# Performance work log

Hardware: AMD Instinct MI355X
Metric: run time of the kernel (lower is better)

## Reference

```python
import jax, jax.numpy as jnp
import numpy as np

B, S = 2, 1024
V, H = 32000, 1024
NH, NKV = 16, 8
HD = H // NH          # 64
L = 8
I = 4 * H             # 4096
EPS = 1e-6
THETA = 10000.0
NEG = -1e9


def setup_inputs() -> dict:
    key = jax.random.key(0)
    ks = jax.random.split(key, 12)
    std = 0.02
    f = lambda k, shape: jax.random.normal(k, shape, jnp.float32) * std
    return {
        "input_ids": jax.random.randint(ks[0], (B, S), 0, V, dtype=jnp.int32),
        "embed": f(ks[1], (V, H)),
        "Wq": f(ks[2], (L, H, NH * HD)),
        "Wk": f(ks[3], (L, H, NKV * HD)),
        "Wv": f(ks[4], (L, H, NKV * HD)),
        "Wo": f(ks[5], (L, NH * HD, H)),
        "Wg": f(ks[6], (L, H, I)),
        "Wu": f(ks[7], (L, H, I)),
        "Wd": f(ks[8], (L, I, H)),
        "ln1": jnp.ones((L, H), jnp.float32),
        "ln2": jnp.ones((L, H), jnp.float32),
        "norm_w": jnp.ones((H,), jnp.float32),
        "lm_head": f(ks[9], (H, V)),
    }


def _rmsnorm(x, w):
    var = jnp.mean(x * x, axis=-1, keepdims=True)
    return x * jax.lax.rsqrt(var + EPS) * w


def _rotate_half(x):
    x1, x2 = jnp.split(x, 2, axis=-1)
    return jnp.concatenate((-x2, x1), axis=-1)


def reference(input_ids, embed, Wq, Wk, Wv, Wo, Wg, Wu, Wd, ln1, ln2, norm_w, lm_head):
    # RoPE tables [S, HD] (freqs duplicated, matching cat((freqs, freqs)))
    inv_freq = 1.0 / (THETA ** (jnp.arange(0, HD, 2, dtype=jnp.float32) / HD))
    t = jnp.arange(S, dtype=jnp.float32)
    freqs = t[:, None] * inv_freq[None, :]
    emb = jnp.concatenate((freqs, freqs), axis=-1)
    cos = jnp.cos(emb)[None, None]  # [1,1,S,HD]
    sin = jnp.sin(emb)[None, None]
    # causal mask [S, S]
    mask = jnp.where(jnp.tril(jnp.ones((S, S), bool)), 0.0, NEG).astype(jnp.float32)

    def layer(h, p):
        wq, wk, wv, wo, wg, wu, wd, g1, g2 = p
        x = _rmsnorm(h, g1)
        q = (x @ wq).reshape(B, S, NH, HD).transpose(0, 2, 1, 3)   # [B,NH,S,HD]
        k = (x @ wk).reshape(B, S, NKV, HD).transpose(0, 2, 1, 3)  # [B,NKV,S,HD]
        v = (x @ wv).reshape(B, S, NKV, HD).transpose(0, 2, 1, 3)
        q = q * cos + _rotate_half(q) * sin
        k = k * cos + _rotate_half(k) * sin
        rep = NH // NKV
        k = jnp.repeat(k, rep, axis=1)  # GQA repeat_interleave
        v = jnp.repeat(v, rep, axis=1)
        scores = jnp.einsum("bhqd,bhkd->bhqk", q, k) / np.sqrt(HD) + mask
        probs = jax.nn.softmax(scores, axis=-1)
        o = jnp.einsum("bhqk,bhkd->bhqd", probs, v)
        o = o.transpose(0, 2, 1, 3).reshape(B, S, NH * HD)
        h = h + o @ wo
        x = _rmsnorm(h, g2)
        h = h + (jax.nn.silu(x @ wg) * (x @ wu)) @ wd
        return h, None

    h = embed[input_ids]  # [B,S,H]
    h, _ = jax.lax.scan(layer, h, (Wq, Wk, Wv, Wo, Wg, Wu, Wd, ln1, ln2))
    h = _rmsnorm(h, norm_w)
    return h @ lm_head  # logits [B,S,V]
```

## Files before the change

kernel.cpp:

```cpp
#include <hip/hip_runtime.h>


typedef unsigned short u16;
typedef __bf16  bf16x8 __attribute__((ext_vector_type(8)));
typedef unsigned short u16x8 __attribute__((ext_vector_type(8)));
typedef float   f32x4  __attribute__((ext_vector_type(4)));

#define DEV static __device__ __forceinline__

constexpr int NB  = 2;
constexpr int S   = 1024;
constexpr int NT  = NB * S;
constexpr int H   = 1024;
constexpr int NH  = 16;
constexpr int NKV = 8;
constexpr int HD  = 64;
constexpr int NL  = 8;
constexpr int FF  = 4096;
constexpr int V   = 32000;
constexpr int QKVW = 2048;

DEV float b2f(u16 x) { return __uint_as_float(((unsigned)x) << 16); }
DEV u16   f2b(float f) {
  unsigned i = __float_as_uint(f);
  return (u16)((i + 0x7fffu + ((i >> 16) & 1u)) >> 16);
}

DEV void gload16(const void* g, void* l) {
  __builtin_amdgcn_global_load_lds(
      (const __attribute__((address_space(1))) void*)g,
      (__attribute__((address_space(3))) void*)l, 16, 0, 0);
}

DEV bf16x8 ld128(const u16* p) { return *reinterpret_cast<const bf16x8*>(p); }

template <int EPI>
__global__ __launch_bounds__(512, 2) void gemm256_k(
    const u16* __restrict__ A, int lda,
    const u16* __restrict__ Bt, int ldb,
    void* __restrict__ C, int ldc, int K)
{
  __shared__ __align__(16) u16 Asm[4][256 * 32];
  __shared__ __align__(16) u16 Bsm[4][256 * 32];

  const int tid  = threadIdx.x;
  const int lane = tid & 63;
  const int lrow = lane & 15;
  const int g    = lane >> 4;
  const int wid  = tid >> 6;
  const int wm   = wid >> 2, wn = wid & 3;

  int flat = blockIdx.y * gridDim.x + blockIdx.x;
  const int cpx = (gridDim.x * gridDim.y) >> 3;
  flat = (flat & 7) * cpx + (flat >> 3);
  const int bx = flat % gridDim.x;
  const int by = flat / gridDim.x;

  const int r0   = tid >> 2, pp = tid & 3;
  const int row1 = 128 + (tid >> 2);
  const int p0 = pp ^ ((r0 ^ (r0 >> 2)) & 3);
  const int p1 = pp ^ ((row1 ^ (row1 >> 2)) & 3);
  const u16* aS0 = A  + (size_t)(bx * 256 + r0)   * lda + p0 * 8;
  const u16* aS1 = A  + (size_t)(bx * 256 + row1) * lda + p1 * 8;
  const u16* bS0 = Bt + (size_t)(by * 256 + r0)   * ldb + p0 * 8;
  const u16* bS1 = Bt + (size_t)(by * 256 + row1) * ldb + p1 * 8;
  const int aB0 = tid * 16, aB1 = (512 + tid) * 16;

  int aOff[8], bOff[4];
  #pragma unroll
  for (int fm = 0; fm < 8; fm++) {
    const int r = wm * 128 + fm * 16 + lrow;
    aOff[fm] = r * 32 + (g ^ ((r ^ (r >> 2)) & 3)) * 8;
  }
  #pragma unroll
  for (int fn = 0; fn < 4; fn++) {
    const int r = wn * 64 + fn * 16 + lrow;
    bOff[fn] = r * 32 + (g ^ ((r ^ (r >> 2)) & 3)) * 8;
  }

  f32x4 acc[8][4] = {};
  const int ntk = K / 32;

  #pragma unroll
  for (int ts = 0; ts < 3; ts++) {
    const long kt = (long)ts * 32;
    gload16(aS0 + kt, (char*)Asm[ts] + aB0);
    gload16(bS0 + kt, (char*)Bsm[ts] + aB0);
    gload16(aS1 + kt, (char*)Asm[ts] + aB1);
    gload16(bS1 + kt, (char*)Bsm[ts] + aB1);
  }
  asm volatile("s_waitcnt vmcnt(8)" ::: "memory");
  __builtin_amdgcn_s_barrier();

#define KTILE(VMW, STG)                                                         \
  {                                                                             \
    const int rs = t & 3, ss = (t + 3) & 3;                                     \
    const long kt = (long)(t + 3) * 32;                                         \
    bf16x8 af[4], bf[4];                                                        \
    _Pragma("unroll") for (int i = 0; i < 4; i++) bf[i] = ld128(&Bsm[rs][bOff[i]]); \
    _Pragma("unroll") for (int i = 0; i < 4; i++) af[i] = ld128(&Asm[rs][aOff[i]]); \
    if (STG) { gload16(aS0 + kt, (char*)Asm[ss] + aB0);                         \
               gload16(bS0 + kt, (char*)Bsm[ss] + aB0); }                       \
    __builtin_amdgcn_s_barrier();                                               \
    asm volatile("s_waitcnt lgkmcnt(0)" ::: "memory");                          \
    __builtin_amdgcn_sched_barrier(0);                                          \
    __builtin_amdgcn_s_setprio(1);                                              \
    _Pragma("unroll") for (int m = 0; m < 4; m++)                               \
      _Pragma("unroll") for (int n = 0; n < 4; n++)                             \
        acc[m][n] = __builtin_amdgcn_mfma_f32_16x16x32_bf16(af[m], bf[n], acc[m][n], 0, 0, 0); \
    __builtin_amdgcn_s_setprio(0);                                              \
    __builtin_amdgcn_s_barrier();                                               \
    _Pragma("unroll") for (int i = 0; i < 4; i++) af[i] = ld128(&Asm[rs][aOff[4 + i]]); \
    if (STG) { gload16(aS1 + kt, (char*)Asm[ss] + aB1);                         \
               gload16(bS1 + kt, (char*)Bsm[ss] + aB1); }                       \
    __builtin_amdgcn_s_barrier();                                               \
    asm volatile("s_waitcnt lgkmcnt(0)" ::: "memory");                          \
    __builtin_amdgcn_sched_barrier(0);                                          \
    __builtin_amdgcn_s_setprio(1);                                              \
    _Pragma("unroll") for (int m = 0; m < 4; m++)                               \
      _Pragma("unroll") for (int n = 0; n < 4; n++)                             \
        acc[4 + m][n] = __builtin_amdgcn_mfma_f32_16x16x32_bf16(af[m], bf[n], acc[4 + m][n], 0, 0, 0); \
    __builtin_amdgcn_s_setprio(0);                                              \
    VMW;                                                                        \
    __builtin_amdgcn_sched_barrier(0);                                          \
    __builtin_amdgcn_s_barrier();                                               \
  }

  {
    int t = 0;
    for (; t < ntk - 3; ++t) KTILE(asm volatile("s_waitcnt vmcnt(8)" ::: "memory"), true);
    KTILE(asm volatile("s_waitcnt vmcnt(4)" ::: "memory"), false); ++t;
    KTILE(asm volatile("s_waitcnt vmcnt(0)" ::: "memory"), false); ++t;
    KTILE((void)0, false);
  }
#undef KTILE

  if (EPI == 2) {
    #pragma unroll
    for (int fm = 0; fm < 8; fm++) {
      #pragma unroll
      for (int fp = 0; fp < 2; fp++) {
        #pragma unroll
        for (int r = 0; r < 4; r++) {
          const size_t row = bx * 256 + wm * 128 + fm * 16 + g * 4 + r;
          const int nb = by * 256 + wn * 64 + fp * 32;
          const int oc = (nb >> 5) * 16 + lrow;
          const float gg = acc[fm][2 * fp][r];
          const float uu = acc[fm][2 * fp + 1][r];
          ((u16*)C)[row * ldc + oc] = f2b(gg / (1.f + __expf(-gg)) * uu);
        }
      }
    }
  } else {
    #pragma unroll
    for (int fm = 0; fm < 8; fm++) {
      #pragma unroll
      for (int fn = 0; fn < 4; fn++) {
        #pragma unroll
        for (int r = 0; r < 4; r++) {
          const size_t row = bx * 256 + wm * 128 + fm * 16 + g * 4 + r;
          const size_t col = by * 256 + wn * 64 + fn * 16 + lrow;
          ((float*)C)[row * ldc + col] = acc[fm][fn][r];
        }
      }
    }
  }
}

template <int BM, int BN, int WM, int WN, int EPI>
__global__ __launch_bounds__(256) void gemm_k(
    const u16* __restrict__ A, int lda,
    const u16* __restrict__ Bt, int ldb,
    void* __restrict__ C, int ldc,
    const float2* __restrict__ tab, int K)
{
  __shared__ __align__(16) u16 As[BM * 32];
  __shared__ __align__(16) u16 Bs[BN * 32];

  const int tid  = threadIdx.x;
  const int lane = tid & 63;
  const int lrow = lane & 15;
  const int kb   = lane >> 4;
  const int w    = tid >> 6;
  const int wm   = w / WN, wn = w % WN;
  constexpr int WR = BM / WM, WC = BN / WN;
  constexpr int FM = WR / 16, FN = WC / 16;

  const u16* Ap = A + blockIdx.x * BM * lda;
  const u16* Bp = Bt + blockIdx.y * BN * ldb;

  f32x4 acc[FM][FN] = {};

  for (int k0 = 0; k0 < K; k0 += 32) {
    #pragma unroll
    for (int i = 0; i < (BM * 4) / 256; i++) {
      const int c = i * 256 + tid;
      gload16(Ap + (c >> 2) * lda + k0 + (c & 3) * 8, (char*)As + c * 16);
    }
    #pragma unroll
    for (int i = 0; i < (BN * 4) / 256; i++) {
      const int c = i * 256 + tid;
      gload16(Bp + (c >> 2) * ldb + k0 + (c & 3) * 8, (char*)Bs + c * 16);
    }
    __syncthreads();

    bf16x8 af[FM], bfv[FN];
    #pragma unroll
    for (int fm = 0; fm < FM; fm++)
      af[fm] = *reinterpret_cast<const bf16x8*>(As + (wm * WR + fm * 16 + lrow) * 32 + kb * 8);
    #pragma unroll
    for (int fn = 0; fn < FN; fn++)
      bfv[fn] = *reinterpret_cast<const bf16x8*>(Bs + (wn * WC + fn * 16 + lrow) * 32 + kb * 8);

    #pragma unroll
    for (int fm = 0; fm < FM; fm++) {
      #pragma unroll
      for (int fn = 0; fn < FN; fn++) {
        acc[fm][fn] = __builtin_amdgcn_mfma_f32_16x16x32_bf16(af[fm], bfv[fn], acc[fm][fn], 0, 0, 0);
      }
    }
    __syncthreads();
  }

  if (EPI == 4) {
    const int colb = blockIdx.y * BN + wn * WC;
    const int head = colb >> 6;
    const float qs = (head < 16) ? 0.125f : 1.0f;
    #pragma unroll
    for (int fm = 0; fm < FM; fm++) {
      #pragma unroll
      for (int r = 0; r < 4; r++) {
        const int row = blockIdx.x * BM + wm * WR + fm * 16 + kb * 4 + r;
        if (head >= 24) {
          #pragma unroll
          for (int fn = 0; fn < FN; fn++)
            ((u16*)C)[row * ldc + colb + fn * 16 + lrow] = f2b(acc[fm][fn][r]);
        } else {
          const int s = row & (S - 1);
          #pragma unroll
          for (int fp = 0; fp < 2; fp++) {
            const int d = fp * 16 + lrow;
            const float2 cs = tab[s * 32 + d];
            const float x1 = acc[fm][fp][r];
            const float x2 = acc[fm][fp + 2][r];
            ((u16*)C)[row * ldc + colb + d]      = f2b((x1 * cs.x - x2 * cs.y) * qs);
            ((u16*)C)[row * ldc + colb + d + 32] = f2b((x2 * cs.x + x1 * cs.y) * qs);
          }
        }
      }
    }
  } else {
    #pragma unroll
    for (int fm = 0; fm < FM; fm++) {
      #pragma unroll
      for (int fn = 0; fn < FN; fn++) {
        #pragma unroll
        for (int r = 0; r < 4; r++) {
          const int row = blockIdx.x * BM + wm * WR + fm * 16 + kb * 4 + r;
          const int col = blockIdx.y * BN + wn * WC + fn * 16 + lrow;
          const float vv = acc[fm][fn][r];
          if (EPI == 0) ((u16*)C)[row * ldc + col] = f2b(vv);
          else          ((float*)C)[row * ldc + col] += vv;
        }
      }
    }
  }
}

__global__ __launch_bounds__(256) void transpose_k(
    const float* __restrict__ W, u16* __restrict__ WT, int K, int N, int rmode,
    size_t wstride, size_t tstride)
{
  __shared__ float t[32][33];
  const float* Wp = W + (size_t)blockIdx.z * wstride;
  u16* WTp = WT + (size_t)blockIdx.z * tstride;
  const int k0 = blockIdx.x * 32, n0 = blockIdx.y * 32;
  const int tx = threadIdx.x & 31, ty = threadIdx.x >> 5;
  #pragma unroll
  for (int i = 0; i < 32; i += 8)
    t[ty + i][tx] = Wp[(size_t)(k0 + ty + i) * N + (n0 + tx)];
  __syncthreads();
  #pragma unroll
  for (int i = 0; i < 32; i += 8) {
    const int n = n0 + ty + i;
    const int orow = (rmode == 0) ? n : ((n >> 4) * 32 + (n & 15) + ((rmode == 2) ? 16 : 0));
    WTp[(size_t)orow * K + (k0 + tx)] = f2b(t[tx][ty + i]);
  }
}

__global__ __launch_bounds__(256) void embed_k(
    const int* __restrict__ ids, const float* __restrict__ E, float* __restrict__ h)
{
  const int t = blockIdx.x;
  const int id = ids[t];
  ((float4*)(h + t * H))[threadIdx.x] = ((const float4*)(E + (size_t)id * H))[threadIdx.x];
}

__global__ __launch_bounds__(256) void rmsnorm_k(
    const float* __restrict__ h, const float* __restrict__ w, u16* __restrict__ x)
{
  const int row = blockIdx.x;
  const float4 hv = ((const float4*)(h + row * H))[threadIdx.x];
  float s = hv.x * hv.x + hv.y * hv.y + hv.z * hv.z + hv.w * hv.w;
  #pragma unroll
  for (int off = 32; off; off >>= 1) s += __shfl_xor(s, off, 64);
  __shared__ float red[4];
  if ((threadIdx.x & 63) == 0) red[threadIdx.x >> 6] = s;
  __syncthreads();
  s = red[0] + red[1] + red[2] + red[3];
  const float scale = rsqrtf(s * (1.f / H) + 1e-6f);
  const float4 wv = ((const float4*)w)[threadIdx.x];
  ushort4 ov;
  ov.x = f2b(hv.x * scale * wv.x);
  ov.y = f2b(hv.y * scale * wv.y);
  ov.z = f2b(hv.z * scale * wv.z);
  ov.w = f2b(hv.w * scale * wv.w);
  ((ushort4*)(x + row * H))[threadIdx.x] = ov;
}

__global__ __launch_bounds__(256) void ropetab_k(float2* __restrict__ tab)
{
  const int idx = blockIdx.x * 256 + threadIdx.x;
  const int s = idx >> 5, d = idx & 31;
  const float ang = s * powf(10000.f, -(2.f * d) / 64.f);
  float sn, cs;
  sincosf(ang, &sn, &cs);
  tab[idx] = make_float2(cs, sn);
}

__global__ __launch_bounds__(256) void fattn_k(
    const u16* __restrict__ qkv, u16* __restrict__ o)
{
  __shared__ __align__(16) u16 Ks[64 * 64];
  __shared__ __align__(16) u16 Vt[64 * 72];
  __shared__ __align__(16) u16 Pw[4][16 * 64];

  const int tid  = threadIdx.x;
  const int lane = tid & 63;
  const int lrow = lane & 15;
  const int g    = lane >> 4;
  const int w    = tid >> 6;
  const int bp = blockIdx.x, by = blockIdx.y;
  const int b = by >> 4, hh = by & 15, kh = hh >> 1;

  for (int half = 0; half < 2; half++) {
    const int bx = half ? (15 - bp) : bp;
    const int q0 = bx * 64;

    bf16x8 aq[2];
    {
      const int qrow = q0 + w * 16 + lrow;
      const u16* qp = qkv + (size_t)(b * S + qrow) * QKVW + hh * 64 + g * 8;
      aq[0] = *reinterpret_cast<const bf16x8*>(qp);
      aq[1] = *reinterpret_cast<const bf16x8*>(qp + 32);
    }

    f32x4 oacc[4] = {};
    float mrow[4], lsum[4];
    #pragma unroll
    for (int r = 0; r < 4; r++) { mrow[r] = -1e30f; lsum[r] = 0.f; }

    const int nt = bx + 1;
    for (int t = 0; t < nt; t++) {
      const int kv0 = t * 64;
      __syncthreads();

      #pragma unroll
      for (int i = 0; i < 2; i++) {
        const int c = i * 256 + tid;
        const int r = c >> 3, p = c & 7;
        gload16(qkv + (size_t)(b * S + kv0 + r) * QKVW + 1024 + kh * 64 + ((p ^ (r & 7)) * 8),
                (char*)Ks + c * 16);
      }
      u16x8 vreg[2];
      #pragma unroll
      for (int i = 0; i < 2; i++) {
        const int c = i * 256 + tid;
        const int k = c >> 3, dch = c & 7;
        vreg[i] = *reinterpret_cast<const u16x8*>(
            qkv + (size_t)(b * S + kv0 + k) * QKVW + 1536 + kh * 64 + dch * 8);
      }
      #pragma unroll
      for (int i = 0; i < 2; i++) {
        const int c = i * 256 + tid;
        const int k = c >> 3, d0 = (c & 7) * 8;
        #pragma unroll
        for (int j = 0; j < 8; j++) {
          const int d = d0 + j;
          Vt[d * 72 + (((k >> 3) ^ (d >> 3)) * 8) + (k & 7)] = vreg[i][j];
        }
      }
      __syncthreads();

      f32x4 sacc[4] = {};
      #pragma unroll
      for (int n = 0; n < 4; n++) {
        const int row = n * 16 + lrow;
        #pragma unroll
        for (int k2 = 0; k2 < 2; k2++) {
          const bf16x8 bk = *reinterpret_cast<const bf16x8*>(
              Ks + row * 64 + (((k2 * 4 + g) ^ (row & 7)) * 8));
          sacc[n] = __builtin_amdgcn_mfma_f32_16x16x32_bf16(aq[k2], bk, sacc[n], 0, 0, 0);
        }
      }

      #pragma unroll
      for (int r = 0; r < 4; r++) {
        const int qglob = q0 + w * 16 + g * 4 + r;
        float sv[4];
        float rm = -1e30f;
        #pragma unroll
        for (int n = 0; n < 4; n++) {
          const int kg = kv0 + n * 16 + lrow;
          sv[n] = (kg <= qglob) ? sacc[n][r] : -1e30f;
          rm = fmaxf(rm, sv[n]);
        }
        #pragma unroll
        for (int mk = 1; mk < 16; mk <<= 1) rm = fmaxf(rm, __shfl_xor(rm, mk, 64));
        const float mnew  = fmaxf(mrow[r], rm);
        const float scale = __expf(mrow[r] - mnew);
        float rs = 0.f;
        u16 pb[4];
        #pragma unroll
        for (int n = 0; n < 4; n++) {
          const float p = __expf(sv[n] - mnew);
          rs += p;
          pb[n] = f2b(p);
        }
        #pragma unroll
        for (int mk = 1; mk < 16; mk <<= 1) rs += __shfl_xor(rs, mk, 64);
        lsum[r] = lsum[r] * scale + rs;
        mrow[r] = mnew;
        #pragma unroll
        for (int dt = 0; dt < 4; dt++) oacc[dt][r] *= scale;
        const int ql = g * 4 + r;
        #pragma unroll
        for (int n = 0; n < 4; n++) {
          const int k = n * 16 + lrow;
          Pw[w][ql * 64 + (((k >> 3) ^ (ql & 7)) * 8) + (k & 7)] = pb[n];
        }
      }

      #pragma unroll
      for (int k2 = 0; k2 < 2; k2++) {
        const bf16x8 pa = *reinterpret_cast<const bf16x8*>(
            &Pw[w][lrow * 64 + (((k2 * 4 + g) ^ (lrow & 7)) * 8)]);
        #pragma unroll
        for (int dt = 0; dt < 4; dt++) {
          const int d = dt * 16 + lrow;
          const bf16x8 vb = *reinterpret_cast<const bf16x8*>(
              &Vt[d * 72 + (((k2 * 4 + g) ^ (d >> 3)) * 8)]);
          oacc[dt] = __builtin_amdgcn_mfma_f32_16x16x32_bf16(pa, vb, oacc[dt], 0, 0, 0);
        }
      }
    }

    #pragma unroll
    for (int dt = 0; dt < 4; dt++) {
      #pragma unroll
      for (int r = 0; r < 4; r++) {
        const int qrow = q0 + w * 16 + g * 4 + r;
        o[(size_t)(b * S + qrow) * H + hh * 64 + dt * 16 + lrow] =
            f2b(oacc[dt][r] / lsum[r]);
      }
    }
  }
}

extern "C" void kernel_launch(void* const* d_in, const int* in_sizes, int n_in,
                              void* d_out, int out_size, void* d_ws, size_t ws_size,
                              hipStream_t stream)
{
  const int*   ids  = (const int*)d_in[0];
  const float* EW   = (const float*)d_in[1];
  const float* Wq   = (const float*)d_in[2];
  const float* Wk   = (const float*)d_in[3];
  const float* Wv   = (const float*)d_in[4];
  const float* Wo   = (const float*)d_in[5];
  const float* Wg   = (const float*)d_in[6];
  const float* Wu   = (const float*)d_in[7];
  const float* Wd   = (const float*)d_in[8];
  const float* ln1  = (const float*)d_in[9];
  const float* ln2  = (const float*)d_in[10];
  const float* nw   = (const float*)d_in[11];
  const float* lmw  = (const float*)d_in[12];
  float* out = (float*)d_out;

  const size_t MB = 1u << 20;
  char* ws = (char*)d_ws;
  float*  h   = (float*)(ws);
  u16*    x   = (u16*)(ws + 8 * MB);
  u16*    qkv = (u16*)(ws + 12 * MB);
  u16*    o   = (u16*)(ws + 20 * MB);
  u16*    ub  = (u16*)(ws + 24 * MB);
  float2* tab = (float2*)(ws + 40 * MB);
  char*   wb  = ws + 41 * MB;

  const size_t sqkv = (size_t)QKVW * H;
  const size_t swo  = (size_t)H * H;
  const size_t sgu  = (size_t)2 * FF * H;
  const size_t swd  = (size_t)H * FF;

  const bool full = ws_size >= 345 * MB;
  if (!full && ws_size < 104 * MB) return;

  u16 *wqkvT, *woT, *wguT, *wdT, *lmT;
  if (full) {
    wqkvT = (u16*)wb;
    woT   = wqkvT + NL * sqkv;
    wguT  = woT + NL * swo;
    wdT   = wguT + NL * sgu;
    lmT   = wdT + NL * swd;
  } else {
    wqkvT = (u16*)wb;
    woT   = wqkvT + sqkv;
    wguT  = woT + swo;
    wdT   = wguT + sgu;
    lmT   = (u16*)wb;
  }

  auto xpose = [&](int l0, int lz, bool dense) {
    const size_t tq = dense ? sqkv : 0, to = dense ? swo : 0;
    const size_t tg = dense ? sgu : 0,  td = dense ? swd : 0;
    transpose_k<<<dim3(H / 32, H / 32, lz), 256, 0, stream>>>(
        Wq + (size_t)l0 * H * H, wqkvT + (size_t)l0 * tq, H, H, 0, (size_t)H * H, tq);
    transpose_k<<<dim3(H / 32, 512 / 32, lz), 256, 0, stream>>>(
        Wk + (size_t)l0 * H * 512, wqkvT + (size_t)l0 * tq + (size_t)1024 * H, H, 512, 0,
        (size_t)H * 512, tq);
    transpose_k<<<dim3(H / 32, 512 / 32, lz), 256, 0, stream>>>(
        Wv + (size_t)l0 * H * 512, wqkvT + (size_t)l0 * tq + (size_t)1536 * H, H, 512, 0,
        (size_t)H * 512, tq);
    transpose_k<<<dim3(H / 32, H / 32, lz), 256, 0, stream>>>(
        Wo + (size_t)l0 * H * H, woT + (size_t)l0 * to, H, H, 0, (size_t)H * H, to);
    transpose_k<<<dim3(H / 32, FF / 32, lz), 256, 0, stream>>>(
        Wg + (size_t)l0 * H * FF, wguT + (size_t)l0 * tg, H, FF, 1, (size_t)H * FF, tg);
    transpose_k<<<dim3(H / 32, FF / 32, lz), 256, 0, stream>>>(
        Wu + (size_t)l0 * H * FF, wguT + (size_t)l0 * tg, H, FF, 2, (size_t)H * FF, tg);
    transpose_k<<<dim3(FF / 32, H / 32, lz), 256, 0, stream>>>(
        Wd + (size_t)l0 * FF * H, wdT + (size_t)l0 * td, FF, H, 0, (size_t)FF * H, td);
  };

  embed_k<<<NT, 256, 0, stream>>>(ids, EW, h);
  ropetab_k<<<(S * 32) / 256, 256, 0, stream>>>(tab);

  if (full) {
    xpose(0, NL, true);
    transpose_k<<<dim3(H / 32, V / 32, 1), 256, 0, stream>>>(lmw, lmT, H, V, 0, 0, 0);
  }

  for (int l = 0; l < NL; l++) {
    if (!full) xpose(l, 1, false);
    u16* pq = wqkvT + (full ? (size_t)l * sqkv : 0);
    u16* po = woT   + (full ? (size_t)l * swo  : 0);
    u16* pg = wguT  + (full ? (size_t)l * sgu  : 0);
    u16* pd = wdT   + (full ? (size_t)l * swd  : 0);

    rmsnorm_k<<<NT, 256, 0, stream>>>(h, ln1 + l * H, x);
    gemm_k<64, 256, 1, 4, 4><<<dim3(NT / 64, QKVW / 256), 256, 0, stream>>>(
        x, H, pq, H, qkv, QKVW, tab, H);
    fattn_k<<<dim3(8, NB * NH), 256, 0, stream>>>(qkv, o);
    gemm_k<64, 128, 1, 4, 1><<<dim3(NT / 64, H / 128), 256, 0, stream>>>(
        o, H, po, H, h, H, nullptr, H);

    rmsnorm_k<<<NT, 256, 0, stream>>>(h, ln2 + l * H, x);
    gemm256_k<2><<<dim3(NT / 256, (2 * FF) / 256), 512, 0, stream>>>(
        x, H, pg, H, ub, FF, H);
    gemm_k<64, 128, 1, 4, 1><<<dim3(NT / 64, H / 128), 256, 0, stream>>>(
        ub, FF, pd, FF, h, H, nullptr, FF);
  }

  rmsnorm_k<<<NT, 256, 0, stream>>>(h, nw, x);
  if (!full)
    transpose_k<<<dim3(H / 32, V / 32, 1), 256, 0, stream>>>(lmw, lmT, H, V, 0, 0, 0);
  gemm256_k<3><<<dim3(NT / 256, V / 256), 512, 0, stream>>>(
      x, H, lmT, H, out, V, H);
}
```

Before: 2.254 ms.

## Fuse residual add into RMSNorm and retile projection GEMMs

The Wo and Wd projection GEMMs now write a bf16 delta buffer instead of read-modify-writing the fp32 residual. A new addnorm kernel adds that delta to the residual and computes the next RMSNorm in one pass, which removes the separate rmsnorm launches and the extra read of h. The GEMM tile shapes change to 64x64 and 64x128 with a different warp layout, giving more blocks on these narrow GEMMs. The trade-off is rounding the residual delta to bf16 before accumulation, plus a slightly larger workspace.

```diff
diff --git a/kernel.cpp b/kernel.cpp
--- a/kernel.cpp
+++ b/kernel.cpp
@@ -258,9 +258,7 @@
         for (int r = 0; r < 4; r++) {
           const int row = blockIdx.x * BM + wm * WR + fm * 16 + kb * 4 + r;
           const int col = blockIdx.y * BN + wn * WC + fn * 16 + lrow;
-          const float vv = acc[fm][fn][r];
-          if (EPI == 0) ((u16*)C)[row * ldc + col] = f2b(vv);
-          else          ((float*)C)[row * ldc + col] += vv;
+          ((u16*)C)[row * ldc + col] = f2b(acc[fm][fn][r]);
         }
       }
     }
@@ -318,6 +316,32 @@
   ((ushort4*)(x + row * H))[threadIdx.x] = ov;
 }
 
+__global__ __launch_bounds__(256) void addnorm_k(
+    float* __restrict__ h, const u16* __restrict__ dl,
+    const float* __restrict__ w, u16* __restrict__ x)
+{
+  const int row = blockIdx.x;
+  float4 hv = ((const float4*)(h + row * H))[threadIdx.x];
+  const ushort4 dv = ((const ushort4*)(dl + row * H))[threadIdx.x];
+  hv.x += b2f(dv.x); hv.y += b2f(dv.y); hv.z += b2f(dv.z); hv.w += b2f(dv.w);
+  ((float4*)(h + row * H))[threadIdx.x] = hv;
+  float s = hv.x * hv.x + hv.y * hv.y + hv.z * hv.z + hv.w * hv.w;
+  #pragma unroll
+  for (int off = 32; off; off >>= 1) s += __shfl_xor(s, off, 64);
+  __shared__ float red[4];
+  if ((threadIdx.x & 63) == 0) red[threadIdx.x >> 6] = s;
+  __syncthreads();
+  s = red[0] + red[1] + red[2] + red[3];
+  const float scale = rsqrtf(s * (1.f / H) + 1e-6f);
+  const float4 wv = ((const float4*)w)[threadIdx.x];
+  ushort4 ov;
+  ov.x = f2b(hv.x * scale * wv.x);
+  ov.y = f2b(hv.y * scale * wv.y);
+  ov.z = f2b(hv.z * scale * wv.z);
+  ov.w = f2b(hv.w * scale * wv.w);
+  ((ushort4*)(x + row * H))[threadIdx.x] = ov;
+}
+
 __global__ __launch_bounds__(256) void ropetab_k(float2* __restrict__ tab)
 {
   const int idx = blockIdx.x * 256 + threadIdx.x;
@@ -492,17 +516,18 @@
   u16*    x   = (u16*)(ws + 8 * MB);
   u16*    qkv = (u16*)(ws + 12 * MB);
   u16*    o   = (u16*)(ws + 20 * MB);
-  u16*    ub  = (u16*)(ws + 24 * MB);
-  float2* tab = (float2*)(ws + 40 * MB);
-  char*   wb  = ws + 41 * MB;
+  u16*    dl  = (u16*)(ws + 24 * MB);
+  u16*    ub  = (u16*)(ws + 28 * MB);
+  float2* tab = (float2*)(ws + 44 * MB);
+  char*   wb  = ws + 45 * MB;
 
   const size_t sqkv = (size_t)QKVW * H;
   const size_t swo  = (size_t)H * H;
   const size_t sgu  = (size_t)2 * FF * H;
   const size_t swd  = (size_t)H * FF;
 
-  const bool full = ws_size >= 345 * MB;
-  if (!full && ws_size < 104 * MB) return;
+  const bool full = ws_size >= 349 * MB;
+  if (!full && ws_size < 108 * MB) return;
 
   u16 *wqkvT, *woT, *wguT, *wdT, *lmT;
   if (full) {
@@ -548,6 +573,8 @@
     transpose_k<<<dim3(H / 32, V / 32, 1), 256, 0, stream>>>(lmw, lmT, H, V, 0, 0, 0);
   }
 
+  rmsnorm_k<<<NT, 256, 0, stream>>>(h, ln1, x);
+
   for (int l = 0; l < NL; l++) {
     if (!full) xpose(l, 1, false);
     u16* pq = wqkvT + (full ? (size_t)l * sqkv : 0);
@@ -555,21 +582,21 @@
     u16* pg = wguT  + (full ? (size_t)l * sgu  : 0);
     u16* pd = wdT   + (full ? (size_t)l * swd  : 0);
 
-    rmsnorm_k<<<NT, 256, 0, stream>>>(h, ln1 + l * H, x);
-    gemm_k<64, 256, 1, 4, 4><<<dim3(NT / 64, QKVW / 256), 256, 0, stream>>>(
+    gemm_k<64, 128, 2, 2, 4><<<dim3(NT / 64, QKVW / 128), 256, 0, stream>>>(
         x, H, pq, H, qkv, QKVW, tab, H);
     fattn_k<<<dim3(8, NB * NH), 256, 0, stream>>>(qkv, o);
-    gemm_k<64, 128, 1, 4, 1><<<dim3(NT / 64, H / 128), 256, 0, stream>>>(
-        o, H, po, H, h, H, nullptr, H);
-
-    rmsnorm_k<<<NT, 256, 0, stream>>>(h, ln2 + l * H, x);
+    gemm_k<64, 64, 2, 2, 0><<<dim3(NT / 64, H / 64), 256, 0, stream>>>(
+        o, H, po, H, dl, H, nullptr, H);
+    addnorm_k<<<NT, 256, 0, stream>>>(h, dl, ln2 + l * H, x);
+
     gemm256_k<2><<<dim3(NT / 256, (2 * FF) / 256), 512, 0, stream>>>(
         x, H, pg, H, ub, FF, H);
-    gemm_k<64, 128, 1, 4, 1><<<dim3(NT / 64, H / 128), 256, 0, stream>>>(
-        ub, FF, pd, FF, h, H, nullptr, FF);
-  }
-
-  rmsnorm_k<<<NT, 256, 0, stream>>>(h, nw, x);
+    gemm_k<64, 64, 2, 2, 0><<<dim3(NT / 64, H / 64), 256, 0, stream>>>(
+        ub, FF, pd, FF, dl, H, nullptr, FF);
+    const float* nxt = (l + 1 < NL) ? (ln1 + (l + 1) * H) : nw;
+    addnorm_k<<<NT, 256, 0, stream>>>(h, dl, nxt, x);
+  }
+
   if (!full)
     transpose_k<<<dim3(H / 32, V / 32, 1), 256, 0, stream>>>(lmw, lmT, H, V, 0, 0, 0);
   gemm256_k<3><<<dim3(NT / 256, V / 256), 512, 0, stream>>>(
```

Result: faster. 2.010 ms (-10.8%).
